# Kernel tuning notes

Hardware: AMD Instinct MI355X
Metric: run time of the kernel (lower is better)

## Reference

```python
import jax, jax.numpy as jnp
import numpy as np

CONF_THRES = 0.596
IOU_THRES = 0.45
CELL_LIMIT = 200   # CELL_SIZE_LIMIT
MAX_CAND = 512     # fixed candidate pool for jit-able NMS
MAX_WH = 4096.0    # per-class NMS box offset (yolov5 trick)
NEG_SLOPE = 0.01   # LeakyReLU default


def xywh2xyxy(b):
    cx, cy, w, h = b[..., 0], b[..., 1], b[..., 2], b[..., 3]
    return jnp.stack([cx - w / 2, cy - h / 2, cx + w / 2, cy + h / 2], axis=-1)


def box_iou(a, b):
    # a:[N,4] b:[M,4] xyxy -> [N,M]
    area_a = (a[:, 2] - a[:, 0]) * (a[:, 3] - a[:, 1])
    area_b = (b[:, 2] - b[:, 0]) * (b[:, 3] - b[:, 1])
    lt = jnp.maximum(a[:, None, :2], b[None, :, :2])
    rb = jnp.minimum(a[:, None, 2:], b[None, :, 2:])
    wh = jnp.clip(rb - lt, 0.0)
    inter = wh[..., 0] * wh[..., 1]
    return inter / (area_a[:, None] + area_b[None, :] - inter + 1e-9)


def nms_single(pred):
    # pred [N,85]: xywh, obj, 80 class probs (yolov5 layout)
    obj = pred[:, 4]
    conf_cls = pred[:, 5:] * obj[:, None]
    conf = conf_cls.max(-1)
    cls = jnp.argmax(conf_cls, -1).astype(jnp.float32)
    box = xywh2xyxy(pred[:, :4])
    score = jnp.where(conf > CONF_THRES, conf, -1.0)
    order = jnp.argsort(-score)[:MAX_CAND]          # top candidates, score-sorted
    boxes, scores, cls = box[order], score[order], cls[order]
    off = boxes + cls[:, None] * MAX_WH             # per-class offset
    iou = box_iou(off, off)
    idx = jnp.arange(MAX_CAND)
    def body(i, keep):
        sup = (iou[i] > IOU_THRES) & (idx > i) & keep[i]
        return keep & ~sup
    keep = jax.lax.fori_loop(0, MAX_CAND, body, scores > 0.0)  # greedy NMS
    ks = jnp.where(keep, scores, -1.0)
    top = jnp.argsort(-ks)[:CELL_LIMIT]
    return boxes[top], ks[top] > 0.0                # [200,4], [200]


def roi_align_1x1(feat, boxes, scale):
    # feat [C,H,W]; boxes [M,4] xyxy image pixels; output_size=1, 2x2 bilinear samples
    C, H, W = feat.shape
    b = boxes * scale
    x1, y1 = b[:, 0], b[:, 1]
    bw = jnp.maximum(b[:, 2] - x1, 1.0)
    bh = jnp.maximum(b[:, 3] - y1, 1.0)
    g = jnp.array([0.25, 0.75], dtype=feat.dtype)   # (i+0.5)/2 sample offsets
    xs = x1[:, None] + g[None, :] * bw[:, None]     # [M,2]
    ys = y1[:, None] + g[None, :] * bh[:, None]
    X = jnp.tile(xs, (1, 2))                        # [M,4] x varies fast
    Y = jnp.repeat(ys, 2, axis=1)
    X = jnp.clip(X, 0.0, W - 1.0)
    Y = jnp.clip(Y, 0.0, H - 1.0)
    x0 = jnp.floor(X).astype(jnp.int32); y0 = jnp.floor(Y).astype(jnp.int32)
    x1i = jnp.minimum(x0 + 1, W - 1); y1i = jnp.minimum(y0 + 1, H - 1)
    wx = X - x0; wy = Y - y0
    v = (feat[:, y0, x0] * ((1 - wy) * (1 - wx))[None]
         + feat[:, y0, x1i] * ((1 - wy) * wx)[None]
         + feat[:, y1i, x0] * (wy * (1 - wx))[None]
         + feat[:, y1i, x1i] * (wy * wx)[None])     # [C,M,4]
    return v.mean(-1).T                             # [M,C]


def reference(out, x1, x2, x3, x4, W1, b1, W2, b2):
    Himg = x1.shape[-2] * 8
    Wimg = x1.shape[-1] * 8
    whwh = jnp.array([Wimg, Himg, Wimg, Himg], dtype=jnp.float32)
    boxes, mask = jax.vmap(nms_single)(out)         # [B,200,4], [B,200]

    def per_img(f1, f2, f3, f4, bb):
        r = jnp.concatenate([
            roi_align_1x1(f1, bb, 1 / 8),
            roi_align_1x1(f2, bb, 1 / 16),
            roi_align_1x1(f3, bb, 1 / 32),
            roi_align_1x1(f4, bb, 1 / 64)], axis=-1)          # [200,1920]
        h = jax.nn.leaky_relu(r @ W1 + b1, NEG_SLOPE)
        h = jax.nn.leaky_relu(h @ W2 + b2, NEG_SLOPE)
        return jnp.concatenate([bb / whwh, h], axis=-1)        # [200,68]

    feats = jax.vmap(per_img)(x1, x2, x3, x4, boxes)
    feats = feats * mask[..., None].astype(feats.dtype)       # zero padded rows
    return feats, mask


def setup_inputs() -> dict:
    key = jax.random.key(0)
    ks = jax.random.split(key, 10)
    B, IMG = 8, 1024
    N = ((IMG // 8) ** 2 + (IMG // 16) ** 2 + (IMG // 32) ** 2) * 3  # 64512
    cxcy = jax.random.uniform(ks[0], (B, N, 2)) * IMG
    wh = jax.random.uniform(ks[1], (B, N, 2)) * 240.0 + 16.0
    obj = jax.random.uniform(ks[2], (B, N, 1))
    cls = jax.random.uniform(ks[3], (B, N, 80))
    out = jnp.concatenate([cxcy, wh, obj, cls], axis=-1)
    x1 = jax.random.normal(ks[4], (B, 128, 128, 128), dtype=jnp.float32)
    x2 = jax.random.normal(ks[5], (B, 256, 64, 64), dtype=jnp.float32)
    x3 = jax.random.normal(ks[6], (B, 512, 32, 32), dtype=jnp.float32)
    x4 = jax.random.normal(ks[7], (B, 1024, 16, 16), dtype=jnp.float32)
    W1 = jax.random.normal(ks[8], (1920, 64)) * 0.02
    b1 = jnp.zeros((64,), jnp.float32)
    W2 = jax.random.normal(ks[9], (64, 64)) * 0.1
    b2 = jnp.zeros((64,), jnp.float32)
    return dict(out=out, x1=x1, x2=x2, x3=x3, x4=x4, W1=W1, b1=b1, W2=W2, b2=b2)
```

## Files before the change

### kernel.cpp

```cpp
#include <hip/hip_runtime.h>
#include <hip/hip_bf16.h>

typedef unsigned int u32;
typedef unsigned long long u64;

#define B_IMG 8
#define N_ANCH 64512
#define NCLS 80
#define ROW 85
#define CONF_T 0.596f
#define IOU_T 0.45f
#define MAXC 512
#define CELL 200
#define CAP 4096

#define SROWS 128
#define SCHUNK_F4 ((SROWS * ROW) / 4)
#define SFULL_ISSUES (SCHUNK_F4 / 64)
#define STAIL (SCHUNK_F4 - SFULL_ISSUES*64)

__device__ __forceinline__ float fsub(float a, float b){ return __fsub_rn(a,b); }
__device__ __forceinline__ float fadd(float a, float b){ return __fadd_rn(a,b); }
__device__ __forceinline__ float fmul(float a, float b){ return __fmul_rn(a,b); }

__device__ __forceinline__ u64 shfl_u64(u64 v, int src) {
    u32 lo = (u32)(v & 0xFFFFFFFFull), hi = (u32)(v >> 32);
    lo = (u32)__shfl((int)lo, src);
    hi = (u32)__shfl((int)hi, src);
    return ((u64)hi << 32) | (u64)lo;
}

__global__ __launch_bounds__(256) void k_score(const float* __restrict__ outp,
                                               float* __restrict__ scores,
                                               u32* __restrict__ hist) {
    __shared__ float srows[SROWS * ROW];

    int blockRow = blockIdx.x * SROWS;
    int tid = threadIdx.x;
    int wave = tid >> 6, lane = tid & 63;

    const float4* src = (const float4*)(outp + (size_t)blockRow * ROW);

    for (int i = wave; i < SFULL_ISSUES; i += 4) {
        __builtin_amdgcn_global_load_lds(
            (const __attribute__((address_space(1))) void*)(src + i * 64 + lane),
            (__attribute__((address_space(3))) void*)((char*)srows + i * 1024),
            16, 0, 0);
    }
    if (tid < STAIL) {
        ((float4*)srows)[SFULL_ISSUES * 64 + tid] = src[SFULL_ISSUES * 64 + tid];
    }
    asm volatile("s_waitcnt vmcnt(0)" ::: "memory");
    __syncthreads();

    int r = tid >> 1;
    int h = tid & 1;
    const float* row = srows + r * ROW;
    float obj = row[4];
    const float* cp = row + 5 + h * 40;
    float m = cp[0];
    #pragma unroll
    for (int c = 1; c < 40; ++c) { float v = cp[c]; m = (v > m) ? v : m; }
    float other = __shfl_xor(m, 1);
    m = (other > m) ? other : m;

    float conf = fmul(m, obj);
    float score = (conf > CONF_T) ? conf : -1.0f;

    if (h == 0) {
        int i = blockRow + r;
        scores[i] = score;
        if (score > 0.0f) {
            u32 key = __float_as_uint(score);
            int b = blockRow / N_ANCH;
            atomicAdd(&hist[(size_t)b * 65536 + (key >> 16)], 1u);
        }
    }
}

__global__ __launch_bounds__(256) void k_thresh(const u32* __restrict__ hist,
                                                u32* __restrict__ thresh) {
    int b = blockIdx.x;
    int tid = threadIdx.x;
    __shared__ u32 csum[256];
    const u32* h = hist + (size_t)b * 65536;
    u32 s = 0;
    for (int i = 0; i < 256; ++i) s += h[tid * 256 + i];
    csum[tid] = s;
    __syncthreads();
    if (tid == 0) {
        u32 cum = 0;
        int ch = 255;
        for (; ch >= 0; --ch) {
            if (cum + csum[ch] >= MAXC) break;
            cum += csum[ch];
        }
        if (ch < 0) { thresh[b] = 0u; return; }
        u32 c2 = cum;
        int bkt = ch * 256 + 255;
        for (; bkt >= ch * 256; --bkt) {
            c2 += h[bkt];
            if (c2 >= MAXC) break;
        }
        thresh[b] = ((u32)bkt) << 16;
    }
}

__global__ __launch_bounds__(256) void k_compact(const float* __restrict__ scores,
                                                 const u32* __restrict__ thresh,
                                                 u32* __restrict__ cnt,
                                                 u64* __restrict__ list) {
    int i = blockIdx.x * blockDim.x + threadIdx.x;
    if (i >= B_IMG * N_ANCH) return;
    float s = scores[i];
    if (s <= 0.0f) return;
    int b = i / N_ANCH;
    u32 key = __float_as_uint(s);
    if (key < thresh[b]) return;
    u32 pos = atomicAdd(&cnt[b], 1u);
    if (pos < CAP) {
        u32 n = (u32)(i - b * N_ANCH);
        list[(size_t)b * CAP + pos] = ((u64)key << 32) | (u64)(0xFFFFFFFFu - n);
    }
}

__global__ __launch_bounds__(512) void k_sort(const float* __restrict__ outp,
                                              const u32* __restrict__ cnt,
                                              const u64* __restrict__ list,
                                              float* __restrict__ oboxw,
                                              float* __restrict__ areaw,
                                              float* __restrict__ bxw,
                                              u32* __restrict__ nvalidw) {
    __shared__ u64 buf[CAP];
    int b = blockIdx.x;
    int tid = threadIdx.x;

    int M = (int)min(cnt[b], (u32)CAP);
    int P = MAXC;
    while (P < M) P <<= 1;

    for (int t = tid; t < P; t += 512)
        buf[t] = (t < M) ? list[(size_t)b * CAP + t] : 0ull;
    __syncthreads();

    for (int k = 2; k <= P; k <<= 1) {
        for (int j = k >> 1; j > 0; j >>= 1) {
            for (int t = tid; t < P; t += 512) {
                int ixj = t ^ j;
                if (ixj > t) {
                    u64 a = buf[t], c = buf[ixj];
                    bool desc = ((t & k) == 0);
                    if (desc ? (a < c) : (a > c)) { buf[t] = c; buf[ixj] = a; }
                }
            }
            __syncthreads();
        }
    }

    int nvalid = min(M, MAXC);
    bool valid = (tid < nvalid);
    u32 n = 0;
    if (valid) n = 0xFFFFFFFFu - (u32)(buf[tid] & 0xFFFFFFFFull);

    float bx0, bx1, bx2, bx3;
    float ob0, ob1, ob2, ob3;
    if (valid) {
        const float* p = outp + ((size_t)b * N_ANCH + n) * ROW;
        float cx = p[0], cy = p[1], w = p[2], h = p[3], obj = p[4];
        float best = -1.0f; int bi = 0;
        for (int c = 0; c < NCLS; ++c) {
            float v = fmul(p[5 + c], obj);
            if (v > best) { best = v; bi = c; }
        }
        float hw = fmul(w, 0.5f), hh = fmul(h, 0.5f);
        bx0 = fsub(cx, hw); bx1 = fsub(cy, hh);
        bx2 = fadd(cx, hw); bx3 = fadd(cy, hh);
        float off = fmul((float)bi, 4096.0f);
        ob0 = fadd(bx0, off); ob1 = fadd(bx1, off);
        ob2 = fadd(bx2, off); ob3 = fadd(bx3, off);
    } else {
        bx0 = bx1 = bx2 = bx3 = 0.0f;
        ob0 = ob1 = ob2 = ob3 = -1.0e6f;
    }
    ((float4*)oboxw)[b * MAXC + tid] = make_float4(ob0, ob1, ob2, ob3);
    areaw[b * MAXC + tid] = fmul(fsub(ob2, ob0), fsub(ob3, ob1));
    ((float4*)bxw)[b * MAXC + tid] = make_float4(bx0, bx1, bx2, bx3);
    if (tid == 0) nvalidw[b] = (u32)nvalid;
}

__global__ __launch_bounds__(64) void k_iou(const float* __restrict__ oboxw,
                                            const float* __restrict__ areaw,
                                            u64* __restrict__ sup) {
    int t = blockIdx.x, b = blockIdx.y;
    int ti = 0;
    while (t >= 8 - ti) { t -= 8 - ti; ++ti; }
    int tj = ti + t;

    int lane = threadIdx.x;
    int i = ti * 64 + lane;
    float4 oi = ((const float4*)oboxw)[b * MAXC + i];
    float ai = areaw[b * MAXC + i];

    __shared__ float jb[5][64];
    int jg = tj * 64 + lane;
    float4 oj = ((const float4*)oboxw)[b * MAXC + jg];
    jb[0][lane] = oj.x; jb[1][lane] = oj.y;
    jb[2][lane] = oj.z; jb[3][lane] = oj.w;
    jb[4][lane] = areaw[b * MAXC + jg];
    __syncthreads();

    u64 bits = 0;
    for (int jl = 0; jl < 64; ++jl) {
        int j = tj * 64 + jl;
        float ltx = fmaxf(oi.x, jb[0][jl]);
        float lty = fmaxf(oi.y, jb[1][jl]);
        float rbx = fminf(oi.z, jb[2][jl]);
        float rby = fminf(oi.w, jb[3][jl]);
        float ww = fmaxf(fsub(rbx, ltx), 0.0f);
        float hh2 = fmaxf(fsub(rby, lty), 0.0f);
        float inter = fmul(ww, hh2);
        float denom = fadd(fsub(fadd(ai, jb[4][jl]), inter), 1e-9f);
        float iou = __fdiv_rn(inter, denom);
        if ((j > i) && (iou > IOU_T)) bits |= (1ull << jl);
    }

    u64* sr = sup + ((size_t)(b * MAXC + i)) * 8;
    if (ti == tj) {
        for (int w = 0; w < ti; ++w) sr[w] = 0ull;
    }
    sr[tj] = bits;
}

#define GW(W, KW, NE, APPLY) \
    { u64 todo = (KW) & (NE); \
      while (todo) { \
          int bb = (int)__builtin_ctzll(todo); \
          const u64* rr = srow + (((W) * 64 + bb) * 8); \
          u64 hm = (bb < 63) ? (~0ull << (bb + 1)) : 0ull; \
          KW &= ~(rr[W] & hm); \
          APPLY \
          todo &= hm & KW; \
      } }

__global__ __launch_bounds__(512) void k_greedy(const u64* __restrict__ sup,
                                                const u32* __restrict__ nvalidw,
                                                const float* __restrict__ bxw,
                                                float* __restrict__ selbox,
                                                u32* __restrict__ selcnt,
                                                float* __restrict__ mask_out) {
    __shared__ u64 srow[MAXC * 8];
    __shared__ u64 neword[8];
    __shared__ u64 keepw[8];
    int b = blockIdx.x;
    int tid = threadIdx.x;
    int nvalid = (int)nvalidw[b];

    const u64* g = sup + (size_t)b * MAXC * 8;
    u64 r0 = g[tid*8+0], r1 = g[tid*8+1], r2 = g[tid*8+2], r3 = g[tid*8+3];
    u64 r4 = g[tid*8+4], r5 = g[tid*8+5], r6 = g[tid*8+6], r7 = g[tid*8+7];
    srow[tid*8+0]=r0; srow[tid*8+1]=r1; srow[tid*8+2]=r2; srow[tid*8+3]=r3;
    srow[tid*8+4]=r4; srow[tid*8+5]=r5; srow[tid*8+6]=r6; srow[tid*8+7]=r7;
    bool ne = ((r0|r1|r2|r3|r4|r5|r6|r7) != 0ull);
    u64 bal = __ballot(ne);
    if ((tid & 63) == 0) neword[tid >> 6] = bal;
    if (tid < 8) {
        int lo = tid * 64;
        u64 kw = 0;
        if (nvalid >= lo + 64) kw = ~0ull;
        else if (nvalid > lo) kw = (1ull << (nvalid - lo)) - 1ull;
        keepw[tid] = kw;
    }
    __syncthreads();

    if (tid == 0) {
        u64 k0=keepw[0], k1=keepw[1], k2=keepw[2], k3=keepw[3];
        u64 k4=keepw[4], k5=keepw[5], k6=keepw[6], k7=keepw[7];
        u64 n0=neword[0], n1=neword[1], n2=neword[2], n3=neword[3];
        u64 n4=neword[4], n5=neword[5], n6=neword[6], n7=neword[7];
        GW(0, k0, n0, k1&=~rr[1]; k2&=~rr[2]; k3&=~rr[3]; k4&=~rr[4]; k5&=~rr[5]; k6&=~rr[6]; k7&=~rr[7];)
        GW(1, k1, n1, k2&=~rr[2]; k3&=~rr[3]; k4&=~rr[4]; k5&=~rr[5]; k6&=~rr[6]; k7&=~rr[7];)
        GW(2, k2, n2, k3&=~rr[3]; k4&=~rr[4]; k5&=~rr[5]; k6&=~rr[6]; k7&=~rr[7];)
        GW(3, k3, n3, k4&=~rr[4]; k5&=~rr[5]; k6&=~rr[6]; k7&=~rr[7];)
        GW(4, k4, n4, k5&=~rr[5]; k6&=~rr[6]; k7&=~rr[7];)
        GW(5, k5, n5, k6&=~rr[6]; k7&=~rr[7];)
        GW(6, k6, n6, k7&=~rr[7];)
        GW(7, k7, n7, )
        keepw[0]=k0; keepw[1]=k1; keepw[2]=k2; keepw[3]=k3;
        keepw[4]=k4; keepw[5]=k5; keepw[6]=k6; keepw[7]=k7;
    }
    __syncthreads();

    int w = tid >> 6, l = tid & 63;
    bool kept = (tid < nvalid) && ((keepw[w] >> l) & 1ull);
    int rank = 0;
    for (int ww = 0; ww < w; ++ww) rank += __popcll(keepw[ww]);
    rank += __popcll(keepw[w] & ((l == 0) ? 0ull : ((1ull << l) - 1ull)));
    if (kept && rank < CELL) {
        float4 bx = ((const float4*)bxw)[b * MAXC + tid];
        float* sb = selbox + ((size_t)b * CELL + rank) * 4;
        sb[0] = bx.x; sb[1] = bx.y; sb[2] = bx.z; sb[3] = bx.w;
        mask_out[b * CELL + rank] = 1.0f;
    }
    if (tid == 0) {
        int tot = 0;
        for (int ww = 0; ww < 8; ++ww) tot += __popcll(keepw[ww]);
        selcnt[b] = (u32)min(tot, CELL);
    }
}

__global__ __launch_bounds__(512) void k_nms(const float* __restrict__ outp,
                                             const u32* __restrict__ cnt,
                                             const u64* __restrict__ list,
                                             float* __restrict__ selbox,
                                             u32* __restrict__ selcnt,
                                             float* __restrict__ mask_out) {
    __shared__ u64 buf[CAP];
    __shared__ float obox[MAXC][4];
    __shared__ float area[MAXC];
    __shared__ u64 keepw[8];
    int b = blockIdx.x;
    int tid = threadIdx.x;

    int M = (int)min(cnt[b], (u32)CAP);
    int P = MAXC;
    while (P < M) P <<= 1;

    for (int t = tid; t < P; t += 512)
        buf[t] = (t < M) ? list[(size_t)b * CAP + t] : 0ull;
    __syncthreads();

    for (int k = 2; k <= P; k <<= 1) {
        for (int j = k >> 1; j > 0; j >>= 1) {
            for (int t = tid; t < P; t += 512) {
                int ixj = t ^ j;
                if (ixj > t) {
                    u64 a = buf[t], c = buf[ixj];
                    bool desc = ((t & k) == 0);
                    if (desc ? (a < c) : (a > c)) { buf[t] = c; buf[ixj] = a; }
                }
            }
            __syncthreads();
        }
    }

    int nvalid = min(M, MAXC);
    bool valid = (tid < nvalid);
    u32 n = 0;
    if (valid) n = 0xFFFFFFFFu - (u32)(buf[tid] & 0xFFFFFFFFull);
    __syncthreads();

    float bx0, bx1, bx2, bx3;
    float ob0, ob1, ob2, ob3;
    if (valid) {
        const float* p = outp + ((size_t)b * N_ANCH + n) * ROW;
        float cx = p[0], cy = p[1], w = p[2], h = p[3], obj = p[4];
        float best = -1.0f; int bi = 0;
        for (int c = 0; c < NCLS; ++c) {
            float v = fmul(p[5 + c], obj);
            if (v > best) { best = v; bi = c; }
        }
        float hw = fmul(w, 0.5f), hh = fmul(h, 0.5f);
        bx0 = fsub(cx, hw); bx1 = fsub(cy, hh);
        bx2 = fadd(cx, hw); bx3 = fadd(cy, hh);
        float off = fmul((float)bi, 4096.0f);
        ob0 = fadd(bx0, off); ob1 = fadd(bx1, off);
        ob2 = fadd(bx2, off); ob3 = fadd(bx3, off);
    } else {
        bx0 = bx1 = bx2 = bx3 = 0.0f;
        ob0 = ob1 = ob2 = ob3 = -1.0e6f;
    }
    obox[tid][0] = ob0; obox[tid][1] = ob1;
    obox[tid][2] = ob2; obox[tid][3] = ob3;
    area[tid] = fmul(fsub(ob2, ob0), fsub(ob3, ob1));
    __syncthreads();

    u64* sup = buf;
    {
        u64 rowb[8] = {0,0,0,0,0,0,0,0};
        float aa = area[tid];
        for (int j = tid + 1; j < MAXC; ++j) {
            float ltx = fmaxf(ob0, obox[j][0]);
            float lty = fmaxf(ob1, obox[j][1]);
            float rbx = fminf(ob2, obox[j][2]);
            float rby = fminf(ob3, obox[j][3]);
            float ww = fmaxf(fsub(rbx, ltx), 0.0f);
            float hh2 = fmaxf(fsub(rby, lty), 0.0f);
            float inter = fmul(ww, hh2);
            float denom = fadd(fsub(fadd(aa, area[j]), inter), 1e-9f);
            float iou = __fdiv_rn(inter, denom);
            if (iou > IOU_T) rowb[j >> 6] |= (1ull << (j & 63));
        }
        for (int w2 = 0; w2 < 8; ++w2) sup[tid * 8 + w2] = rowb[w2];
    }
    __syncthreads();

    if (tid < 64) {
        int lane = tid;
        u64 kw = 0;
        if (lane < 8) {
            int lo = lane * 64;
            if (nvalid >= lo + 64) kw = ~0ull;
            else if (nvalid > lo) kw = (1ull << (nvalid - lo)) - 1ull;
        }
        for (int i = 0; i < MAXC; ++i) {
            u64 wv = shfl_u64(kw, i >> 6);
            if ((wv >> (i & 63)) & 1ull) {
                if (lane < 8) kw &= ~sup[(size_t)i * 8 + lane];
            }
        }
        if (lane < 8) keepw[lane] = kw;
    }
    __syncthreads();

    int w = tid >> 6, l = tid & 63;
    bool kept = valid && ((keepw[w] >> l) & 1ull);
    int rank = 0;
    for (int ww = 0; ww < w; ++ww) rank += __popcll(keepw[ww]);
    rank += __popcll(keepw[w] & ((l == 0) ? 0ull : ((1ull << l) - 1ull)));
    if (kept && rank < CELL) {
        float* sb = selbox + ((size_t)b * CELL + rank) * 4;
        sb[0] = bx0; sb[1] = bx1; sb[2] = bx2; sb[3] = bx3;
        mask_out[b * CELL + rank] = 1.0f;
    }
    if (tid == 0) {
        int tot = 0;
        for (int ww = 0; ww < 8; ++ww) tot += __popcll(keepw[ww]);
        selcnt[b] = (u32)min(tot, CELL);
    }
}

__global__ __launch_bounds__(256) void k_roi_gather(
        const float* __restrict__ x1, const float* __restrict__ x2,
        const float* __restrict__ x3, const float* __restrict__ x4,
        const float* __restrict__ selbox, const u32* __restrict__ selcnt,
        float* __restrict__ rws) {
    int slot = blockIdx.y;
    int b = blockIdx.z;
    if (slot >= (int)selcnt[b]) return;

    int unit = blockIdx.x * 256 + threadIdx.x;
    int c = unit >> 2;
    int p = unit & 3;

    const float* fb; int Wd; float s; int cl;
    if (c < 128)      { fb = x1 + (size_t)b * 128 * 128 * 128; Wd = 128; s = 0.125f;    cl = c; }
    else if (c < 384) { fb = x2 + (size_t)b * 256 * 64 * 64;   Wd = 64;  s = 0.0625f;   cl = c - 128; }
    else if (c < 896) { fb = x3 + (size_t)b * 512 * 32 * 32;   Wd = 32;  s = 0.03125f;  cl = c - 384; }
    else              { fb = x4 + (size_t)b * 1024 * 16 * 16;  Wd = 16;  s = 0.015625f; cl = c - 896; }

    const float* sb = selbox + ((size_t)b * CELL + slot) * 4;
    float box0 = sb[0], box1 = sb[1], box2 = sb[2], box3 = sb[3];

    float bx1f = box0 * s, by1f = box1 * s;
    float bw = fmaxf(box2 * s - bx1f, 1.0f);
    float bh = fmaxf(box3 * s - by1f, 1.0f);
    float gx = (p & 1)  ? 0.75f : 0.25f;
    float gy = (p >> 1) ? 0.75f : 0.25f;
    float X = bx1f + gx * bw;
    float Y = by1f + gy * bh;
    X = fminf(fmaxf(X, 0.0f), (float)(Wd - 1));
    Y = fminf(fmaxf(Y, 0.0f), (float)(Wd - 1));
    int x0 = (int)floorf(X), y0 = (int)floorf(Y);
    int x1i = min(x0 + 1, Wd - 1), y1i = min(y0 + 1, Wd - 1);
    float wx = X - (float)x0, wy = Y - (float)y0;

    const float* f = fb + (size_t)cl * Wd * Wd;
    float v = f[y0 * Wd + x0]  * ((1.0f - wy) * (1.0f - wx))
            + f[y0 * Wd + x1i] * ((1.0f - wy) * wx)
            + f[y1i * Wd + x0] * (wy * (1.0f - wx))
            + f[y1i * Wd + x1i]* (wy * wx);

    int lane = threadIdx.x & 63;
    int base = lane & ~3;
    float v0 = __shfl(v, base + 0);
    float v1 = __shfl(v, base + 1);
    float v2 = __shfl(v, base + 2);
    float v3 = __shfl(v, base + 3);
    if (p == 0) {
        rws[((size_t)b * CELL + slot) * 1920 + c] = (((v0 + v1) + v2) + v3) * 0.25f;
    }
}

__global__ __launch_bounds__(256) void k_mlp(
        const float* __restrict__ W1, const float* __restrict__ b1,
        const float* __restrict__ W2, const float* __restrict__ b2,
        const float* __restrict__ selbox, const u32* __restrict__ selcnt,
        const float* __restrict__ rws, float* __restrict__ feats) {
    int slot = blockIdx.x;
    int b = blockIdx.y;
    if (slot >= (int)selcnt[b]) return;
    int tid = threadIdx.x;

    __shared__ float psum[4][64];
    __shared__ float h1[64];

    const float* r = rws + ((size_t)b * CELL + slot) * 1920;

    int j = tid & 63, part = tid >> 6;
    {
        float acc = 0.0f;
        int k0 = part * 480;
        for (int k = k0; k < k0 + 480; ++k)
            acc += r[k] * W1[(size_t)k * 64 + j];
        psum[part][j] = acc;
    }
    __syncthreads();
    if (tid < 64) {
        float v = psum[0][tid] + psum[1][tid] + psum[2][tid] + psum[3][tid] + b1[tid];
        h1[tid] = (v >= 0.0f) ? v : 0.01f * v;
    }
    __syncthreads();

    float* orow = feats + ((size_t)b * CELL + slot) * 68;
    if (tid < 64) {
        float acc = b2[tid];
        for (int k = 0; k < 64; ++k) acc += h1[k] * W2[k * 64 + tid];
        float v = (acc >= 0.0f) ? acc : 0.01f * acc;
        orow[4 + tid] = v;
    }
    if (tid < 4) {
        const float* sb = selbox + ((size_t)b * CELL + slot) * 4;
        orow[tid] = sb[tid] * (1.0f / 1024.0f);
    }
}

__global__ __launch_bounds__(256) void k_roi_mlp(
        const float* __restrict__ x1, const float* __restrict__ x2,
        const float* __restrict__ x3, const float* __restrict__ x4,
        const float* __restrict__ W1, const float* __restrict__ b1,
        const float* __restrict__ W2, const float* __restrict__ b2,
        const float* __restrict__ selbox, const u32* __restrict__ selcnt,
        float* __restrict__ feats) {
    int slot = blockIdx.x;
    int b = blockIdx.y;
    if (slot >= (int)selcnt[b]) return;
    int tid = threadIdx.x;

    __shared__ float r[1920];
    __shared__ float psum[4][64];
    __shared__ float h1[64];

    const float* sb = selbox + ((size_t)b * CELL + slot) * 4;
    float box0 = sb[0], box1 = sb[1], box2 = sb[2], box3 = sb[3];

    const float* feat[4] = {
        x1 + (size_t)b * 128 * 128 * 128,
        x2 + (size_t)b * 256 * 64 * 64,
        x3 + (size_t)b * 512 * 32 * 32,
        x4 + (size_t)b * 1024 * 16 * 16
    };
    const int   Cs[4]  = {128, 256, 512, 1024};
    const int   Wd_[4] = {128, 64, 32, 16};
    const float Ss[4]  = {0.125f, 0.0625f, 0.03125f, 0.015625f};
    const int   Off[4] = {0, 128, 384, 896};

    for (int lvl = 0; lvl < 4; ++lvl) {
        int Wd = Wd_[lvl], C = Cs[lvl];
        float s = Ss[lvl];
        float bx1f = box0 * s, by1f = box1 * s;
        float bw = fmaxf(box2 * s - bx1f, 1.0f);
        float bh = fmaxf(box3 * s - by1f, 1.0f);
        float xs[2] = { bx1f + 0.25f * bw, bx1f + 0.75f * bw };
        float ys[2] = { by1f + 0.25f * bh, by1f + 0.75f * bh };
        int idx[4][4]; float wt[4][4];
        for (int p = 0; p < 4; ++p) {
            float X = xs[p & 1], Y = ys[p >> 1];
            X = fminf(fmaxf(X, 0.0f), (float)(Wd - 1));
            Y = fminf(fmaxf(Y, 0.0f), (float)(Wd - 1));
            int x0 = (int)floorf(X), y0 = (int)floorf(Y);
            int x1i = min(x0 + 1, Wd - 1), y1i = min(y0 + 1, Wd - 1);
            float wx = X - (float)x0, wy = Y - (float)y0;
            idx[p][0] = y0 * Wd + x0;  idx[p][1] = y0 * Wd + x1i;
            idx[p][2] = y1i * Wd + x0; idx[p][3] = y1i * Wd + x1i;
            wt[p][0] = (1.0f - wy) * (1.0f - wx); wt[p][1] = (1.0f - wy) * wx;
            wt[p][2] = wy * (1.0f - wx);          wt[p][3] = wy * wx;
        }
        const float* fb = feat[lvl];
        int HW = Wd * Wd;
        for (int c = tid; c < C; c += 256) {
            const float* f = fb + (size_t)c * HW;
            float acc = 0.0f;
            for (int p = 0; p < 4; ++p)
                acc += f[idx[p][0]] * wt[p][0] + f[idx[p][1]] * wt[p][1]
                     + f[idx[p][2]] * wt[p][2] + f[idx[p][3]] * wt[p][3];
            r[Off[lvl] + c] = acc * 0.25f;
        }
    }
    __syncthreads();

    int j = tid & 63, part = tid >> 6;
    {
        float acc = 0.0f;
        int k0 = part * 480;
        for (int k = k0; k < k0 + 480; ++k)
            acc += r[k] * W1[(size_t)k * 64 + j];
        psum[part][j] = acc;
    }
    __syncthreads();
    if (tid < 64) {
        float v = psum[0][tid] + psum[1][tid] + psum[2][tid] + psum[3][tid] + b1[tid];
        h1[tid] = (v >= 0.0f) ? v : 0.01f * v;
    }
    __syncthreads();

    float* orow = feats + ((size_t)b * CELL + slot) * 68;
    if (tid < 64) {
        float acc = b2[tid];
        for (int k = 0; k < 64; ++k) acc += h1[k] * W2[k * 64 + tid];
        float v = (acc >= 0.0f) ? acc : 0.01f * acc;
        orow[4 + tid] = v;
    }
    if (tid < 4) {
        float bv = (tid == 0) ? box0 : (tid == 1) ? box1 : (tid == 2) ? box2 : box3;
        orow[tid] = bv * (1.0f / 1024.0f);
    }
}

extern "C" void kernel_launch(void* const* d_in, const int* in_sizes, int n_in,
                              void* d_out, int out_size, void* d_ws, size_t ws_size,
                              hipStream_t stream) {
    const float* outp = (const float*)d_in[0];
    const float* x1 = (const float*)d_in[1];
    const float* x2 = (const float*)d_in[2];
    const float* x3 = (const float*)d_in[3];
    const float* x4 = (const float*)d_in[4];
    const float* W1 = (const float*)d_in[5];
    const float* b1 = (const float*)d_in[6];
    const float* W2 = (const float*)d_in[7];
    const float* b2 = (const float*)d_in[8];

    char* ws = (char*)d_ws;
    const size_t o_hist   = 0;
    const size_t o_cnt    = 2097152;
    const size_t o_thresh = 2097152 + 256;
    const size_t o_scores = 2097152 + 512;
    const size_t o_list   = o_scores + 2064384;
    const size_t o_selbox = o_list + 262144;
    const size_t o_selcnt = o_selbox + 25600;
    const size_t o_rws    = o_selcnt + 256;
    const size_t ws_need_rws = o_rws + (size_t)B_IMG * CELL * 1920 * 4;
    const size_t o_sup    = ws_need_rws;
    const size_t o_obox   = o_sup + 262144;
    const size_t o_area   = o_obox + 65536;
    const size_t o_bx     = o_area + 16384;
    const size_t o_nvalid = o_bx + 65536;
    const size_t ws_need_full = o_nvalid + 256;

    u32*   hist   = (u32*)(ws + o_hist);
    u32*   cnt    = (u32*)(ws + o_cnt);
    u32*   thresh = (u32*)(ws + o_thresh);
    float* scores = (float*)(ws + o_scores);
    u64*   list   = (u64*)(ws + o_list);
    float* selbox = (float*)(ws + o_selbox);
    u32*   selcnt = (u32*)(ws + o_selcnt);
    float* rws    = (float*)(ws + o_rws);
    u64*   sup    = (u64*)(ws + o_sup);
    float* oboxw  = (float*)(ws + o_obox);
    float* areaw  = (float*)(ws + o_area);
    float* bxw    = (float*)(ws + o_bx);
    u32*   nvalidw= (u32*)(ws + o_nvalid);

    float* feats = (float*)d_out;
    float* mask  = feats + (size_t)B_IMG * CELL * 68;

    hipMemsetAsync(d_out, 0, (size_t)out_size * sizeof(float), stream);
    hipMemsetAsync(ws, 0, 2097152 + 512, stream);

    int total = B_IMG * N_ANCH;
    int score_blocks = total / SROWS;
    int blocks = (total + 255) / 256;
    k_score  <<<score_blocks, 256, 0, stream>>>(outp, scores, hist);
    k_thresh <<<B_IMG, 256, 0, stream>>>(hist, thresh);
    k_compact<<<blocks, 256, 0, stream>>>(scores, thresh, cnt, list);

    if (ws_size >= ws_need_full) {
        k_sort  <<<B_IMG, 512, 0, stream>>>(outp, cnt, list, oboxw, areaw, bxw, nvalidw);
        k_iou   <<<dim3(36, B_IMG), 64, 0, stream>>>(oboxw, areaw, sup);
        k_greedy<<<B_IMG, 512, 0, stream>>>(sup, nvalidw, bxw, selbox, selcnt, mask);
    } else {
        k_nms   <<<B_IMG, 512, 0, stream>>>(outp, cnt, list, selbox, selcnt, mask);
    }

    if (ws_size >= ws_need_rws) {
        k_roi_gather<<<dim3(30, CELL, B_IMG), 256, 0, stream>>>(
            x1, x2, x3, x4, selbox, selcnt, rws);
        k_mlp<<<dim3(CELL, B_IMG), 256, 0, stream>>>(
            W1, b1, W2, b2, selbox, selcnt, rws, feats);
    } else {
        k_roi_mlp<<<dim3(CELL, B_IMG), 256, 0, stream>>>(
            x1, x2, x3, x4, W1, b1, W2, b2, selbox, selcnt, feats);
    }
}
```

Before: 378.8 us.

## Make score kernel persistent with double-buffered LDS chunk staging

Converts k_score from one block per 128 rows into a persistent grid of 768 blocks that loop over 64-row chunks. Each block prefetches the next chunk into a second LDS buffer with global_load_lds while it reduces the current one, using partial vmcnt waits. The class max is also split four ways per row instead of two. This is meant to hide global load latency on the streaming read of the prediction tensor. The cost is hand-tuned waitcnt counts that depend on how many loads each wave issues, which is fragile if the chunk size changes.

```diff
diff --git a/kernel.cpp b/kernel.cpp
--- a/kernel.cpp
+++ b/kernel.cpp
@@ -14,10 +14,12 @@
 #define CELL 200
 #define CAP 4096
 
-#define SROWS 128
-#define SCHUNK_F4 ((SROWS * ROW) / 4)
-#define SFULL_ISSUES (SCHUNK_F4 / 64)
-#define STAIL (SCHUNK_F4 - SFULL_ISSUES*64)
+#define CROWS 64
+#define CWORDS (CROWS * ROW)
+#define CBYTES (CWORDS * 4)
+#define CF16   (CBYTES / 1024)
+#define NCHUNK (B_IMG * N_ANCH / CROWS)
+#define SGRID  768
 
 __device__ __forceinline__ float fsub(float a, float b){ return __fsub_rn(a,b); }
 __device__ __forceinline__ float fadd(float a, float b){ return __fadd_rn(a,b); }
@@ -30,51 +32,71 @@
     return ((u64)hi << 32) | (u64)lo;
 }
 
+__device__ __forceinline__ void stage_chunk(const float* __restrict__ outp,
+                                            int chunk, float* dst,
+                                            int wave, int lane) {
+    const char* gbase = (const char*)outp + (size_t)chunk * CBYTES;
+    char* lbase = (char*)dst;
+    for (int i = wave; i < CF16; i += 4) {
+        __builtin_amdgcn_global_load_lds(
+            (const __attribute__((address_space(1))) void*)(gbase + i * 1024 + lane * 16),
+            (__attribute__((address_space(3))) void*)(lbase + i * 1024),
+            16, 0, 0);
+    }
+    if (wave == 1) {
+        __builtin_amdgcn_global_load_lds(
+            (const __attribute__((address_space(1))) void*)(gbase + CF16 * 1024 + lane * 4),
+            (__attribute__((address_space(3))) void*)(lbase + CF16 * 1024),
+            4, 0, 0);
+    }
+}
+
 __global__ __launch_bounds__(256) void k_score(const float* __restrict__ outp,
                                                float* __restrict__ scores,
                                                u32* __restrict__ hist) {
-    __shared__ float srows[SROWS * ROW];
-
-    int blockRow = blockIdx.x * SROWS;
+    __shared__ float srows[2][CWORDS];
+
     int tid = threadIdx.x;
     int wave = tid >> 6, lane = tid & 63;
-
-    const float4* src = (const float4*)(outp + (size_t)blockRow * ROW);
-
-    for (int i = wave; i < SFULL_ISSUES; i += 4) {
-        __builtin_amdgcn_global_load_lds(
-            (const __attribute__((address_space(1))) void*)(src + i * 64 + lane),
-            (__attribute__((address_space(3))) void*)((char*)srows + i * 1024),
-            16, 0, 0);
-    }
-    if (tid < STAIL) {
-        ((float4*)srows)[SFULL_ISSUES * 64 + tid] = src[SFULL_ISSUES * 64 + tid];
-    }
-    asm volatile("s_waitcnt vmcnt(0)" ::: "memory");
-    __syncthreads();
-
-    int r = tid >> 1;
-    int h = tid & 1;
-    const float* row = srows + r * ROW;
-    float obj = row[4];
-    const float* cp = row + 5 + h * 40;
-    float m = cp[0];
-    #pragma unroll
-    for (int c = 1; c < 40; ++c) { float v = cp[c]; m = (v > m) ? v : m; }
-    float other = __shfl_xor(m, 1);
-    m = (other > m) ? other : m;
-
-    float conf = fmul(m, obj);
-    float score = (conf > CONF_T) ? conf : -1.0f;
-
-    if (h == 0) {
-        int i = blockRow + r;
-        scores[i] = score;
-        if (score > 0.0f) {
-            u32 key = __float_as_uint(score);
-            int b = blockRow / N_ANCH;
-            atomicAdd(&hist[(size_t)b * 65536 + (key >> 16)], 1u);
-        }
+    int lr = tid >> 2;
+    int q  = tid & 3;
+
+    stage_chunk(outp, blockIdx.x, srows[0], wave, lane);
+
+    int cur = 0;
+    for (int c = blockIdx.x; c < NCHUNK; c += SGRID) {
+        int cn = c + SGRID;
+        bool hasNext = (cn < NCHUNK);
+        if (hasNext) {
+            stage_chunk(outp, cn, srows[cur ^ 1], wave, lane);
+            if (wave < 2) asm volatile("s_waitcnt vmcnt(6)" ::: "memory");
+            else          asm volatile("s_waitcnt vmcnt(5)" ::: "memory");
+        } else {
+            asm volatile("s_waitcnt vmcnt(0)" ::: "memory");
+        }
+        __builtin_amdgcn_s_barrier();
+
+        const float* row = srows[cur] + lr * ROW;
+        float obj = row[4];
+        const float* cp = row + 5 + q * 20;
+        float m = cp[0];
+        #pragma unroll
+        for (int k = 1; k < 20; ++k) { float v = cp[k]; m = (v > m) ? v : m; }
+        float o1 = __shfl_xor(m, 1); m = (o1 > m) ? o1 : m;
+        float o2 = __shfl_xor(m, 2); m = (o2 > m) ? o2 : m;
+
+        float conf = fmul(m, obj);
+        float score = (conf > CONF_T) ? conf : -1.0f;
+        if (q == 0) {
+            int gi = c * CROWS + lr;
+            scores[gi] = score;
+            if (score > 0.0f) {
+                int b = c / (N_ANCH / CROWS);
+                atomicAdd(&hist[(size_t)b * 65536 + (__float_as_uint(score) >> 16)], 1u);
+            }
+        }
+        __builtin_amdgcn_s_barrier();
+        cur ^= 1;
     }
 }
 
@@ -667,9 +689,8 @@
     hipMemsetAsync(ws, 0, 2097152 + 512, stream);
 
     int total = B_IMG * N_ANCH;
-    int score_blocks = total / SROWS;
     int blocks = (total + 255) / 256;
-    k_score  <<<score_blocks, 256, 0, stream>>>(outp, scores, hist);
+    k_score  <<<SGRID, 256, 0, stream>>>(outp, scores, hist);
     k_thresh <<<B_IMG, 256, 0, stream>>>(hist, thresh);
     k_compact<<<blocks, 256, 0, stream>>>(scores, thresh, cnt, list);
 
```

Measured after the change: 382.3 us. No clear change (+0.9%).
